# Performance work log

Hardware: AMD Instinct MI355X
Metric: run time of the kernel (lower is better)

The kernel has to match this reference:

```python
import jax, jax.numpy as jnp
import numpy as np

B, P, J, MOT, K, NB, WN, H = 64, 12273, 80, 94, 64, 20, 17, 128
W_POSE = 1.0

def euler_to_rotmat(a):
    # a: [..., 3] radians, R = Rz @ Ry @ Rx
    sx, sy, sz = jnp.sin(a[..., 0]), jnp.sin(a[..., 1]), jnp.sin(a[..., 2])
    cx, cy, cz = jnp.cos(a[..., 0]), jnp.cos(a[..., 1]), jnp.cos(a[..., 2])
    r00 = cz * cy; r01 = cz * sy * sx - sz * cx; r02 = cz * sy * cx + sz * sx
    r10 = sz * cy; r11 = sz * sy * sx + cz * cx; r12 = sz * sy * cx - cz * sx
    r20 = -sy;     r21 = cy * sx;                r22 = cy * cx
    return jnp.stack([jnp.stack([r00, r01, r02], -1),
                      jnp.stack([r10, r11, r12], -1),
                      jnp.stack([r20, r21, r22], -1)], -2)

def setup_inputs() -> dict:
    key = jax.random.key(0)
    ks = jax.random.split(key, 20)
    f32 = jnp.float32
    return {
        'in_pc_batch': jax.random.normal(ks[0], (B, P, 3), f32),
        't_nor': jax.random.normal(ks[1], (B, P, 3), f32),
        'rest_verts': jax.random.normal(ks[2], (P, 3), f32),
        'skin_weights': jax.random.uniform(ks[3], (P, J), f32),
        'mul_weight_list': jax.random.normal(ks[4], (J, MOT), f32),
        'query': jax.random.normal(ks[5], (B, J, 3), f32),
        'cloth_pose_std': jax.random.uniform(ks[6], (3,), f32),
        'cloth_pose_mean': jax.random.normal(ks[7], (3,), f32),
        'cloth_trans_std': jax.random.uniform(ks[8], (3,), f32),
        'cloth_trans_mean': jax.random.normal(ks[9], (3,), f32),
        'W1': jax.random.normal(ks[10], (3 + K, H), f32) * 0.1,
        'b1': jnp.zeros((H,), f32),
        'W2': jax.random.normal(ks[11], (H, 6), f32) * 0.1,
        'b2': jnp.zeros((6,), f32),
        'tmtemp': jax.random.normal(ks[12], (B, MOT, K), f32),
        'Wd': jax.random.normal(ks[13], (MOT * K, NB * WN), f32) * 0.02,
        'bd': jnp.zeros((NB * WN,), f32),
        'DPSD': jax.random.normal(ks[14], (NB, WN, P, 3), f32) * 0.1,
        'ssdr_res_std': jax.random.uniform(ks[15], (3,), f32),
        'ssdr_res_mean': jax.random.normal(ks[16], (3,), f32),
    }

def reference(in_pc_batch, t_nor, rest_verts, skin_weights, mul_weight_list,
              query, cloth_pose_std, cloth_pose_mean, cloth_trans_std,
              cloth_trans_mean, W1, b1, W2, b2, tmtemp, Wd, bd, DPSD,
              ssdr_res_std, ssdr_res_mean):
    # per-joint field input: [B, J, K]
    field_input = jnp.einsum('bjk,lj->blk', tmtemp, jax.nn.relu(mul_weight_list))
    # FieldNet: per-joint MLP on concat(query, field_input) -> [B, J, 6]
    h = jnp.concatenate([query, field_input], axis=-1)
    pred_rt = jax.nn.relu(h @ W1 + b1) @ W2 + b2
    pred_pose = pred_rt[..., 0:3] * cloth_pose_std + cloth_pose_mean
    pred_trans = (query + pred_rt[..., 3:6]) * cloth_trans_std + cloth_trans_mean
    # detailsnet + fused 20-basis accumulation: [B, P, 3]
    nbat = tmtemp.shape[0]
    detailkey = (tmtemp.reshape(nbat, -1) @ Wd + bd).reshape(nbat, NB, WN)
    detail_res = jnp.einsum('bnw,nwpx->bpx', detailkey, DPSD)
    detail_res = detail_res * ssdr_res_std + ssdr_res_mean
    # SSDR LBS skinning with Euler-angle rotations (degrees -> radians)
    R = euler_to_rotmat(jnp.deg2rad(pred_pose))            # [B, J, 3, 3]
    skinned = (jnp.einsum('pj,bjxy,py->bpx', skin_weights, R, rest_verts)
               + jnp.einsum('pj,bjx->bpx', skin_weights, pred_trans))
    out_pc = skinned + detail_res                          # [B, P, 3]
    loss_pose_l1 = jnp.mean(jnp.abs(in_pc_batch[:, :, 0:3] - out_pc))
    loss = loss_pose_l1 * W_POSE + 1e-4 * jnp.mean(DPSD ** 2)
    return loss[None], out_pc
```

## Files before the change

### kernel.cpp

```cpp
#include <hip/hip_runtime.h>

#define B_   64
#define P_   12273
#define J_   80
#define MOT_ 94
#define K_   64
#define H_   128
#define Q_   340
#define NE_  36819
#define MK_  6016
#define PW_  12288

typedef float v4f  __attribute__((ext_vector_type(4)));
typedef float v8f  __attribute__((ext_vector_type(8)));
typedef float v16f __attribute__((ext_vector_type(16)));
#define AS4 __attribute__((address_space(4)))

__device__ __forceinline__ const AS4 float* unif(const float* p){
  return (const AS4 float*)(unsigned long long)p;
}
__device__ __forceinline__ const AS4 v4f* univ4(const float* p){
  return (const AS4 v4f*)(unsigned long long)p;
}
__device__ __forceinline__ const AS4 v8f* univ8(const float* p){
  return (const AS4 v8f*)(unsigned long long)p;
}
__device__ __forceinline__ const AS4 v16f* univ16(const float* p){
  return (const AS4 v16f*)(unsigned long long)p;
}

__global__ __launch_bounds__(256) void k_prep(
    const float* __restrict__ query, const float* __restrict__ mwl,
    const float* __restrict__ tm,    const float* __restrict__ W1,
    const float* __restrict__ b1,    const float* __restrict__ W2,
    const float* __restrict__ b2,    const float* __restrict__ cps,
    const float* __restrict__ cpm,   const float* __restrict__ cts,
    const float* __restrict__ ctm,   const float* __restrict__ skin,
    float* __restrict__ G,           float* __restrict__ tm_t,
    float* __restrict__ w_t,         float* __restrict__ lacc)
{
  __shared__ float smem[80 * 65];
  int blk = blockIdx.x;
  int t = threadIdx.x;
  if (blk < 1280){
    int lane = t & 63;
    int wid = __builtin_amdgcn_readfirstlane(t >> 6);
    int bj = blk * 4 + wid;
    int b = bj / J_, l = bj - b * J_;
    float* hs = smem + wid * 80;
    float acc = 0.f;
    const AS4 float* mp = unif(mwl + l * MOT_);
    const float* tp = tm + (size_t)b * MK_ + lane;
    #pragma unroll 2
    for (int j = 0; j < MOT_; j++){
      float w = mp[j]; w = w > 0.f ? w : 0.f;
      acc = fmaf(w, tp[j * K_], acc);
    }
    hs[3 + lane] = acc;
    if (lane < 3) hs[lane] = query[(size_t)bj * 3 + lane];
    __syncthreads();
    float a1 = b1[lane], a2 = b1[lane + 64];
    for (int i = 0; i < 3 + K_; i++){
      float hv = hs[i];
      a1 = fmaf(hv, W1[i * H_ + lane], a1);
      a2 = fmaf(hv, W1[i * H_ + 64 + lane], a2);
    }
    a1 = a1 > 0.f ? a1 : 0.f;
    a2 = a2 > 0.f ? a2 : 0.f;
    const AS4 float* b2c = unif(b2);
    float rt[6];
    #pragma unroll
    for (int o = 0; o < 6; o++){
      float po = fmaf(a1, W2[lane * 6 + o], a2 * W2[(lane + 64) * 6 + o]);
      #pragma unroll
      for (int off = 32; off; off >>= 1) po += __shfl_xor(po, off);
      rt[o] = po + b2c[o];
    }
    const float D2R = 0.017453292519943295f;
    float ax = fmaf(rt[0], cps[0], cpm[0]) * D2R;
    float ay = fmaf(rt[1], cps[1], cpm[1]) * D2R;
    float az = fmaf(rt[2], cps[2], cpm[2]) * D2R;
    float tx = fmaf(hs[0] + rt[3], cts[0], ctm[0]);
    float ty = fmaf(hs[1] + rt[4], cts[1], ctm[1]);
    float tz = fmaf(hs[2] + rt[5], cts[2], ctm[2]);
    float sx, cx, sy, cy, sz, cz;
    sincosf(ax, &sx, &cx); sincosf(ay, &sy, &cy); sincosf(az, &sz, &cz);
    if (lane == 0){
      float4 r0 = make_float4(cz*cy, cz*sy*sx - sz*cx, cz*sy*cx + sz*sx, tx);
      float4 r1 = make_float4(sz*cy, sz*sy*sx + cz*cx, sz*sy*cx - cz*sx, ty);
      float4 r2 = make_float4(-sy,   cy*sx,            cy*cx,            tz);
      float4* g = (float4*)(G + (size_t)bj * 12);
      g[0] = r0; g[1] = r1; g[2] = r2;
    }
  } else if (blk < 1374){
    int m0 = (blk - 1280) * 64;
    int ml = t & 63, g = t >> 6;
    #pragma unroll
    for (int r = 0; r < 16; r++){
      int b = g * 16 + r;
      smem[ml * 65 + b] = tm[(size_t)b * MK_ + m0 + ml];
    }
    __syncthreads();
    int bl = t & 63;
    #pragma unroll
    for (int r = 0; r < 16; r++){
      int m = g * 16 + r;
      tm_t[(size_t)(m0 + m) * 64 + bl] = smem[m * 65 + bl];
    }
  } else if (blk < 1566){
    int p0 = (blk - 1374) * 64;
    #pragma unroll
    for (int k = 0; k < 20; k++){
      int idx = k * 256 + t;
      int pl = idx / 80, j = idx - pl * 80;
      int p = p0 + pl;
      smem[j * 65 + pl] = (p < P_) ? skin[(size_t)p * J_ + j] : 0.f;
    }
    __syncthreads();
    #pragma unroll
    for (int k = 0; k < 20; k++){
      int idx = k * 256 + t;
      int j = idx >> 6, pl = idx & 63;
      w_t[(size_t)j * PW_ + p0 + pl] = smem[j * 65 + pl];
    }
  } else {
    if (t < 2) lacc[t] = 0.f;
  }
}

__global__ __launch_bounds__(256) void k_dkey(
    const float* __restrict__ tm_t, const float* __restrict__ Wd,
    float* __restrict__ part)
{
  int t = threadIdx.x;
  int lane = t & 63;
  int wid = __builtin_amdgcn_readfirstlane(t >> 6);
  int qt = blockIdx.x;
  int q = qt * 64 + lane;
  bool vq = q < Q_;
  int m0 = blockIdx.y * 64;
  const AS4 v16f* tr = univ16(tm_t);
  float acc[16];
  #pragma unroll
  for (int i = 0; i < 16; i++) acc[i] = 0.f;
  float wbuf[4];
  #pragma unroll
  for (int i = 0; i < 4; i++)
    wbuf[i] = vq ? Wd[(size_t)(m0 + i) * Q_ + q] : 0.f;
  v16f tb0 = tr[(size_t)(m0 + 0) * 4 + wid];
  v16f tb1 = tr[(size_t)(m0 + 1) * 4 + wid];
  #pragma unroll 4
  for (int mm = 0; mm < 60; mm++){
    float wd = wbuf[mm & 3];
    wbuf[mm & 3] = vq ? Wd[(size_t)(m0 + mm + 4) * Q_ + q] : 0.f;
    v16f tv = tb0; tb0 = tb1;
    tb1 = tr[(size_t)(m0 + mm + 2) * 4 + wid];
    #pragma unroll
    for (int i = 0; i < 16; i++) acc[i] = fmaf(tv[i], wd, acc[i]);
  }
  #pragma unroll
  for (int mm = 60; mm < 64; mm++){
    float wd = wbuf[mm & 3];
    v16f tv = tb0; tb0 = tb1;
    if (mm < 62) tb1 = tr[(size_t)(m0 + mm + 2) * 4 + wid];
    #pragma unroll
    for (int i = 0; i < 16; i++) acc[i] = fmaf(tv[i], wd, acc[i]);
  }
  float* pb = part + ((size_t)blockIdx.y * 6 + qt) * 4096 + (size_t)(wid * 16) * 64;
  #pragma unroll
  for (int i = 0; i < 16; i++) pb[i * 64 + lane] = acc[i];
}

__global__ __launch_bounds__(256) void k_dkred(
    const float* __restrict__ part, const float* __restrict__ bd,
    float* __restrict__ dk_t, int S)
{
  int t = threadIdx.x;
  int jj = blockIdx.x * 32 + (t >> 3);
  int dl = t & 7;
  int b = jj / Q_, q = jj - b * Q_;
  int qt = q >> 6, ql = q & 63;
  const float* pp = part + (size_t)qt * 4096 + b * 64 + ql;
  float s = 0.f;
  for (int d = dl; d < S; d += 8) s += pp[(size_t)d * 6 * 4096];
  s += __shfl_xor(s, 1); s += __shfl_xor(s, 2); s += __shfl_xor(s, 4);
  if (dl == 0) dk_t[q * 64 + b] = bd[q] + s;
}

__device__ __forceinline__ void dconsume(const AS4 v16f* dkv, int qa, int wid,
                                         const float* dc, float* acc,
                                         float& sq, bool doSq)
{
  v16f r0 = dkv[(qa + 0) * 4 + wid];
  v16f r1 = dkv[(qa + 1) * 4 + wid];
  v16f r2 = dkv[(qa + 2) * 4 + wid];
  v16f r3 = dkv[(qa + 3) * 4 + wid];
  v16f r4 = dkv[(qa + 4) * 4 + wid];
  if (doSq){
    #pragma unroll
    for (int i = 0; i < 5; i++) sq = fmaf(dc[i], dc[i], sq);
  }
  #pragma unroll
  for (int i = 0; i < 16; i++){
    acc[i] = fmaf(r0[i], dc[0], acc[i]);
    acc[i] = fmaf(r1[i], dc[1], acc[i]);
    acc[i] = fmaf(r2[i], dc[2], acc[i]);
    acc[i] = fmaf(r3[i], dc[3], acc[i]);
    acc[i] = fmaf(r4[i], dc[4], acc[i]);
  }
}

__global__ __launch_bounds__(256) void k_detail(
    const float* __restrict__ DPSD, const float* __restrict__ dk_t,
    float* __restrict__ stg0, float* __restrict__ out,
    float* __restrict__ lacc, int qn)
{
  int t = threadIdx.x;
  int lane = t & 63;
  int wid = __builtin_amdgcn_readfirstlane(t >> 6);
  int b0 = wid * 16;
  int e = blockIdx.x * 64 + lane;
  bool ve = e < NE_;
  int q0 = blockIdx.y * qn;
  const AS4 v16f* dkv = univ16(dk_t);
  const float* Dp = DPSD + (ve ? e : 0);
  float acc[16];
  #pragma unroll
  for (int i = 0; i < 16; i++) acc[i] = 0.f;
  float sq = 0.f;
  bool doSq = (wid == 0);
  float da[5], db[5];
  #pragma unroll
  for (int i = 0; i < 5; i++) da[i] = Dp[(size_t)(q0 + i) * NE_];
  #pragma unroll
  for (int i = 0; i < 5; i++) db[i] = Dp[(size_t)(q0 + 5 + i) * NE_];
  int ng = qn / 5;
  int g = 0;
  for (; g + 2 < ng; g += 2){
    int qa = q0 + g * 5;
    float ta[5], tb[5];
    #pragma unroll
    for (int i = 0; i < 5; i++) ta[i] = Dp[(size_t)(qa + 10 + i) * NE_];
    dconsume(dkv, qa, wid, da, acc, sq, doSq);
    #pragma unroll
    for (int i = 0; i < 5; i++) da[i] = ta[i];
    #pragma unroll
    for (int i = 0; i < 5; i++) tb[i] = Dp[(size_t)(qa + 15 + i) * NE_];
    dconsume(dkv, qa + 5, wid, db, acc, sq, doSq);
    #pragma unroll
    for (int i = 0; i < 5; i++) db[i] = tb[i];
  }
  dconsume(dkv, q0 + (ng - 2) * 5, wid, da, acc, sq, doSq);
  dconsume(dkv, q0 + (ng - 1) * 5, wid, db, acc, sq, doSq);
  if (ve){
    bool toOut = (blockIdx.y + 1 == gridDim.y);
    float* dst = toOut ? (out + 1 + e) : (stg0 + e);
    #pragma unroll
    for (int i = 0; i < 16; i++)
      dst[(size_t)(b0 + i) * NE_] = acc[i];
  }
  if (doSq){
    if (!ve) sq = 0.f;
    #pragma unroll
    for (int off = 32; off; off >>= 1) sq += __shfl_xor(sq, off);
    if (lane == 0) atomicAdd(&lacc[1], sq);
  }
}

__global__ __launch_bounds__(256) void k_skin(
    const float* __restrict__ G, const float* __restrict__ w_t,
    const float* __restrict__ rest, const float* __restrict__ in_pc,
    const float* __restrict__ stg0, const float* __restrict__ rstd,
    const float* __restrict__ rmean,
    float* __restrict__ out, float* __restrict__ lacc, int two)
{
  int t = threadIdx.x;
  int lane = t & 63;
  int wid = __builtin_amdgcn_readfirstlane(t >> 6);
  int p  = blockIdx.x * 64 + lane;
  int bA = blockIdx.y * 8 + wid * 2;
  const AS4 v4f* gA = univ4(G + (size_t)bA * J_ * 12);
  const AS4 v4f* gB = univ4(G + ((size_t)bA + 1) * J_ * 12);
  float accA[12], accB[12];
  #pragma unroll
  for (int c = 0; c < 12; c++){ accA[c] = 0.f; accB[c] = 0.f; }
  const float* wp = w_t + p;
  #pragma unroll 4
  for (int j = 0; j < J_; j++){
    float w = wp[(size_t)j * PW_];
    v4f a0 = gA[j * 3 + 0], a1 = gA[j * 3 + 1], a2 = gA[j * 3 + 2];
    v4f c0 = gB[j * 3 + 0], c1 = gB[j * 3 + 1], c2 = gB[j * 3 + 2];
    #pragma unroll
    for (int c = 0; c < 4; c++){
      accA[c]     = fmaf(w, a0[c], accA[c]);
      accA[4 + c] = fmaf(w, a1[c], accA[4 + c]);
      accA[8 + c] = fmaf(w, a2[c], accA[8 + c]);
      accB[c]     = fmaf(w, c0[c], accB[c]);
      accB[4 + c] = fmaf(w, c1[c], accB[4 + c]);
      accB[8 + c] = fmaf(w, c2[c], accB[8 + c]);
    }
  }
  bool vp = p < P_;
  float vx = 0.f, vy = 0.f, vz = 0.f;
  if (vp){ vx = rest[p * 3]; vy = rest[p * 3 + 1]; vz = rest[p * 3 + 2]; }
  float srs[3], srm[3];
  #pragma unroll
  for (int x = 0; x < 3; x++){ srs[x] = rstd[x]; srm[x] = rmean[x]; }
  float lsum = 0.f;
  if (vp){
    size_t baseA = ((size_t)bA * P_ + p) * 3;
    size_t baseB = baseA + (size_t)P_ * 3;
    #pragma unroll
    for (int x = 0; x < 3; x++){
      float det = out[1 + baseA + x];
      if (two) det += stg0[baseA + x];
      float v = fmaf(accA[x*4+0], vx, fmaf(accA[x*4+1], vy, fmaf(accA[x*4+2], vz, accA[x*4+3])));
      v += fmaf(det, srs[x], srm[x]);
      lsum += fabsf(in_pc[baseA + x] - v);
      out[1 + baseA + x] = v;
    }
    #pragma unroll
    for (int x = 0; x < 3; x++){
      float det = out[1 + baseB + x];
      if (two) det += stg0[baseB + x];
      float v = fmaf(accB[x*4+0], vx, fmaf(accB[x*4+1], vy, fmaf(accB[x*4+2], vz, accB[x*4+3])));
      v += fmaf(det, srs[x], srm[x]);
      lsum += fabsf(in_pc[baseB + x] - v);
      out[1 + baseB + x] = v;
    }
  }
  #pragma unroll
  for (int off = 32; off; off >>= 1) lsum += __shfl_xor(lsum, off);
  __shared__ float red[4];
  if (lane == 0) red[wid] = lsum;
  __syncthreads();
  if (t == 0) atomicAdd(&lacc[0], red[0] + red[1] + red[2] + red[3]);
}

__global__ void k_finalize(const float* __restrict__ lacc, float* __restrict__ out){
  if (threadIdx.x == 0 && blockIdx.x == 0){
    float loss = lacc[0] * (1.f / 2356416.f) + 1e-4f * (lacc[1] * (1.f / 12518460.f));
    out[0] = loss;
  }
}

extern "C" void kernel_launch(void* const* d_in, const int* in_sizes, int n_in,
                              void* d_out, int out_size, void* d_ws, size_t ws_size,
                              hipStream_t stream){
  const float* in_pc = (const float*)d_in[0];
  const float* rest  = (const float*)d_in[2];
  const float* skin  = (const float*)d_in[3];
  const float* mwl   = (const float*)d_in[4];
  const float* query = (const float*)d_in[5];
  const float* cps   = (const float*)d_in[6];
  const float* cpm   = (const float*)d_in[7];
  const float* cts   = (const float*)d_in[8];
  const float* ctm   = (const float*)d_in[9];
  const float* W1    = (const float*)d_in[10];
  const float* b1    = (const float*)d_in[11];
  const float* W2    = (const float*)d_in[12];
  const float* b2    = (const float*)d_in[13];
  const float* tm    = (const float*)d_in[14];
  const float* Wd    = (const float*)d_in[15];
  const float* bd    = (const float*)d_in[16];
  const float* DPSD  = (const float*)d_in[17];
  const float* rstd  = (const float*)d_in[18];
  const float* rmean = (const float*)d_in[19];
  float* out = (float*)d_out;

  float* ws   = (float*)d_ws;
  float* G    = ws;
  float* dk_t = G + 61440;
  float* lacc = dk_t + 21760;
  float* tm_t = lacc + 64;
  float* w_t  = tm_t + 385024;
  float* un   = w_t + 983040;

  size_t have = ws_size / 4;
  int nqh = (have >= (size_t)(1451328 + 2356416)) ? 2 : 1;
  int qn = Q_ / nqh;

  k_prep    <<<1567, 256, 0, stream>>>(query, mwl, tm, W1, b1, W2, b2,
                                       cps, cpm, cts, ctm, skin,
                                       G, tm_t, w_t, lacc);
  k_dkey    <<<dim3(6, 94), 256, 0, stream>>>(tm_t, Wd, un);
  k_dkred   <<<680, 256, 0, stream>>>(un, bd, dk_t, 94);
  k_detail  <<<dim3(576, nqh), 256, 0, stream>>>(DPSD, dk_t, un, out, lacc, qn);
  k_skin    <<<dim3(192, 8), 256, 0, stream>>>(G, w_t, rest, in_pc, un, rstd, rmean,
                                               out, lacc, nqh - 1);
  k_finalize<<<1, 64, 0, stream>>>(lacc, out);
}
```

Before: 255.5 us.

## Relayout detail keys and rotation buffers; software-prefetch loads in prep MLP

Detail keys are now stored per 16-batch group, contiguous over q, so each wave in k_detail streams its slice with simpler scalar addressing. The per-joint transform buffer G interleaves batch pairs so k_skin reads both batches' matrices from one contiguous stream. In k_prep, the motion-weight and W1 loops use an 8-deep register prefetch ring to hide global load latency. Together these aim to cut address overhead and load stalls, at the cost of more registers and tighter coupling of layouts between kernels.

```diff
diff --git a/kernel.cpp b/kernel.cpp
--- a/kernel.cpp
+++ b/kernel.cpp
@@ -10,9 +10,9 @@
 #define NE_  36819
 #define MK_  6016
 #define PW_  12288
+#define STG_ 2356416
 
 typedef float v4f  __attribute__((ext_vector_type(4)));
-typedef float v8f  __attribute__((ext_vector_type(8)));
 typedef float v16f __attribute__((ext_vector_type(16)));
 #define AS4 __attribute__((address_space(4)))
 
@@ -21,9 +21,6 @@
 }
 __device__ __forceinline__ const AS4 v4f* univ4(const float* p){
   return (const AS4 v4f*)(unsigned long long)p;
-}
-__device__ __forceinline__ const AS4 v8f* univ8(const float* p){
-  return (const AS4 v8f*)(unsigned long long)p;
 }
 __device__ __forceinline__ const AS4 v16f* univ16(const float* p){
   return (const AS4 v16f*)(unsigned long long)p;
@@ -51,19 +48,36 @@
     float acc = 0.f;
     const AS4 float* mp = unif(mwl + l * MOT_);
     const float* tp = tm + (size_t)b * MK_ + lane;
-    #pragma unroll 2
+    float tbuf[8];
+    #pragma unroll
+    for (int s = 0; s < 8; s++) tbuf[s] = tp[s * K_];
+    #pragma unroll 8
     for (int j = 0; j < MOT_; j++){
+      float tv = tbuf[j & 7];
+      if (j + 8 < MOT_) tbuf[j & 7] = tp[(j + 8) * K_];
       float w = mp[j]; w = w > 0.f ? w : 0.f;
-      acc = fmaf(w, tp[j * K_], acc);
+      acc = fmaf(w, tv, acc);
     }
     hs[3 + lane] = acc;
     if (lane < 3) hs[lane] = query[(size_t)bj * 3 + lane];
     __syncthreads();
     float a1 = b1[lane], a2 = b1[lane + 64];
-    for (int i = 0; i < 3 + K_; i++){
+    float wa[8], wb[8];
+    #pragma unroll
+    for (int s = 0; s < 8; s++){
+      wa[s] = W1[s * H_ + lane];
+      wb[s] = W1[s * H_ + 64 + lane];
+    }
+    #pragma unroll 8
+    for (int i = 0; i < 67; i++){
       float hv = hs[i];
-      a1 = fmaf(hv, W1[i * H_ + lane], a1);
-      a2 = fmaf(hv, W1[i * H_ + 64 + lane], a2);
+      float va = wa[i & 7], vb = wb[i & 7];
+      if (i + 8 < 67){
+        wa[i & 7] = W1[(i + 8) * H_ + lane];
+        wb[i & 7] = W1[(i + 8) * H_ + 64 + lane];
+      }
+      a1 = fmaf(hv, va, a1);
+      a2 = fmaf(hv, vb, a2);
     }
     a1 = a1 > 0.f ? a1 : 0.f;
     a2 = a2 > 0.f ? a2 : 0.f;
@@ -89,7 +103,8 @@
       float4 r0 = make_float4(cz*cy, cz*sy*sx - sz*cx, cz*sy*cx + sz*sx, tx);
       float4 r1 = make_float4(sz*cy, sz*sy*sx + cz*cx, sz*sy*cx - cz*sx, ty);
       float4 r2 = make_float4(-sy,   cy*sx,            cy*cx,            tz);
-      float4* g = (float4*)(G + (size_t)bj * 12);
+      size_t o = ((size_t)(b >> 1) * J_ + l) * 24 + (b & 1) * 12;
+      float4* g = (float4*)(G + o);
       g[0] = r0; g[1] = r1; g[2] = r2;
     }
   } else if (blk < 1374){
@@ -173,7 +188,7 @@
 
 __global__ __launch_bounds__(256) void k_dkred(
     const float* __restrict__ part, const float* __restrict__ bd,
-    float* __restrict__ dk_t, int S)
+    float* __restrict__ dk_s, int S)
 {
   int t = threadIdx.x;
   int jj = blockIdx.x * 32 + (t >> 3);
@@ -184,18 +199,19 @@
   float s = 0.f;
   for (int d = dl; d < S; d += 8) s += pp[(size_t)d * 6 * 4096];
   s += __shfl_xor(s, 1); s += __shfl_xor(s, 2); s += __shfl_xor(s, 4);
-  if (dl == 0) dk_t[q * 64 + b] = bd[q] + s;
-}
-
-__device__ __forceinline__ void dconsume(const AS4 v16f* dkv, int qa, int wid,
-                                         const float* dc, float* acc,
-                                         float& sq, bool doSq)
-{
-  v16f r0 = dkv[(qa + 0) * 4 + wid];
-  v16f r1 = dkv[(qa + 1) * 4 + wid];
-  v16f r2 = dkv[(qa + 2) * 4 + wid];
-  v16f r3 = dkv[(qa + 3) * 4 + wid];
-  v16f r4 = dkv[(qa + 4) * 4 + wid];
+  if (dl == 0)
+    dk_s[(size_t)(b >> 4) * (Q_ * 16) + q * 16 + (b & 15)] = bd[q] + s;
+}
+
+__device__ __forceinline__ void dk_consume(const AS4 v16f* dkv, int qa,
+                                           const float* dc, float* acc,
+                                           float& sq, bool doSq)
+{
+  v16f r0 = dkv[qa + 0];
+  v16f r1 = dkv[qa + 1];
+  v16f r2 = dkv[qa + 2];
+  v16f r3 = dkv[qa + 3];
+  v16f r4 = dkv[qa + 4];
   if (doSq){
     #pragma unroll
     for (int i = 0; i < 5; i++) sq = fmaf(dc[i], dc[i], sq);
@@ -211,8 +227,8 @@
 }
 
 __global__ __launch_bounds__(256) void k_detail(
-    const float* __restrict__ DPSD, const float* __restrict__ dk_t,
-    float* __restrict__ stg0, float* __restrict__ out,
+    const float* __restrict__ DPSD, const float* __restrict__ dk_s,
+    float* __restrict__ stg, float* __restrict__ out,
     float* __restrict__ lacc, int qn)
 {
   int t = threadIdx.x;
@@ -222,39 +238,38 @@
   int e = blockIdx.x * 64 + lane;
   bool ve = e < NE_;
   int q0 = blockIdx.y * qn;
-  const AS4 v16f* dkv = univ16(dk_t);
+  const AS4 v16f* dkv = univ16(dk_s + (size_t)wid * (Q_ * 16));
   const float* Dp = DPSD + (ve ? e : 0);
   float acc[16];
   #pragma unroll
   for (int i = 0; i < 16; i++) acc[i] = 0.f;
   float sq = 0.f;
   bool doSq = (wid == 0);
+  int ng = qn / 5;
   float da[5], db[5];
   #pragma unroll
   for (int i = 0; i < 5; i++) da[i] = Dp[(size_t)(q0 + i) * NE_];
   #pragma unroll
   for (int i = 0; i < 5; i++) db[i] = Dp[(size_t)(q0 + 5 + i) * NE_];
-  int ng = qn / 5;
-  int g = 0;
-  for (; g + 2 < ng; g += 2){
+  for (int g = 0; g + 2 < ng; g += 2){
     int qa = q0 + g * 5;
     float ta[5], tb[5];
     #pragma unroll
     for (int i = 0; i < 5; i++) ta[i] = Dp[(size_t)(qa + 10 + i) * NE_];
-    dconsume(dkv, qa, wid, da, acc, sq, doSq);
+    dk_consume(dkv, qa, da, acc, sq, doSq);
     #pragma unroll
     for (int i = 0; i < 5; i++) da[i] = ta[i];
     #pragma unroll
     for (int i = 0; i < 5; i++) tb[i] = Dp[(size_t)(qa + 15 + i) * NE_];
-    dconsume(dkv, qa + 5, wid, db, acc, sq, doSq);
+    dk_consume(dkv, qa + 5, db, acc, sq, doSq);
     #pragma unroll
     for (int i = 0; i < 5; i++) db[i] = tb[i];
   }
-  dconsume(dkv, q0 + (ng - 2) * 5, wid, da, acc, sq, doSq);
-  dconsume(dkv, q0 + (ng - 1) * 5, wid, db, acc, sq, doSq);
+  dk_consume(dkv, q0 + (ng - 2) * 5, da, acc, sq, doSq);
+  dk_consume(dkv, q0 + (ng - 1) * 5, db, acc, sq, doSq);
   if (ve){
     bool toOut = (blockIdx.y + 1 == gridDim.y);
-    float* dst = toOut ? (out + 1 + e) : (stg0 + e);
+    float* dst = toOut ? (out + 1 + e) : (stg + e);
     #pragma unroll
     for (int i = 0; i < 16; i++)
       dst[(size_t)(b0 + i) * NE_] = acc[i];
@@ -270,7 +285,7 @@
 __global__ __launch_bounds__(256) void k_skin(
     const float* __restrict__ G, const float* __restrict__ w_t,
     const float* __restrict__ rest, const float* __restrict__ in_pc,
-    const float* __restrict__ stg0, const float* __restrict__ rstd,
+    const float* __restrict__ stg, const float* __restrict__ rstd,
     const float* __restrict__ rmean,
     float* __restrict__ out, float* __restrict__ lacc, int two)
 {
@@ -279,8 +294,8 @@
   int wid = __builtin_amdgcn_readfirstlane(t >> 6);
   int p  = blockIdx.x * 64 + lane;
   int bA = blockIdx.y * 8 + wid * 2;
-  const AS4 v4f* gA = univ4(G + (size_t)bA * J_ * 12);
-  const AS4 v4f* gB = univ4(G + ((size_t)bA + 1) * J_ * 12);
+  int bp = (blockIdx.y * 4 + wid);
+  const AS4 v4f* gS = univ4(G + (size_t)bp * J_ * 24);
   float accA[12], accB[12];
   #pragma unroll
   for (int c = 0; c < 12; c++){ accA[c] = 0.f; accB[c] = 0.f; }
@@ -288,8 +303,8 @@
   #pragma unroll 4
   for (int j = 0; j < J_; j++){
     float w = wp[(size_t)j * PW_];
-    v4f a0 = gA[j * 3 + 0], a1 = gA[j * 3 + 1], a2 = gA[j * 3 + 2];
-    v4f c0 = gB[j * 3 + 0], c1 = gB[j * 3 + 1], c2 = gB[j * 3 + 2];
+    v4f a0 = gS[j * 6 + 0], a1 = gS[j * 6 + 1], a2 = gS[j * 6 + 2];
+    v4f c0 = gS[j * 6 + 3], c1 = gS[j * 6 + 4], c2 = gS[j * 6 + 5];
     #pragma unroll
     for (int c = 0; c < 4; c++){
       accA[c]     = fmaf(w, a0[c], accA[c]);
@@ -313,7 +328,7 @@
     #pragma unroll
     for (int x = 0; x < 3; x++){
       float det = out[1 + baseA + x];
-      if (two) det += stg0[baseA + x];
+      if (two) det += stg[baseA + x];
       float v = fmaf(accA[x*4+0], vx, fmaf(accA[x*4+1], vy, fmaf(accA[x*4+2], vz, accA[x*4+3])));
       v += fmaf(det, srs[x], srm[x]);
       lsum += fabsf(in_pc[baseA + x] - v);
@@ -322,7 +337,7 @@
     #pragma unroll
     for (int x = 0; x < 3; x++){
       float det = out[1 + baseB + x];
-      if (two) det += stg0[baseB + x];
+      if (two) det += stg[baseB + x];
       float v = fmaf(accB[x*4+0], vx, fmaf(accB[x*4+1], vy, fmaf(accB[x*4+2], vz, accB[x*4+3])));
       v += fmaf(det, srs[x], srm[x]);
       lsum += fabsf(in_pc[baseB + x] - v);
@@ -370,8 +385,8 @@
 
   float* ws   = (float*)d_ws;
   float* G    = ws;
-  float* dk_t = G + 61440;
-  float* lacc = dk_t + 21760;
+  float* dk_s = G + 61440;
+  float* lacc = dk_s + 21760;
   float* tm_t = lacc + 64;
   float* w_t  = tm_t + 385024;
   float* un   = w_t + 983040;
@@ -384,8 +399,8 @@
                                        cps, cpm, cts, ctm, skin,
                                        G, tm_t, w_t, lacc);
   k_dkey    <<<dim3(6, 94), 256, 0, stream>>>(tm_t, Wd, un);
-  k_dkred   <<<680, 256, 0, stream>>>(un, bd, dk_t, 94);
-  k_detail  <<<dim3(576, nqh), 256, 0, stream>>>(DPSD, dk_t, un, out, lacc, qn);
+  k_dkred   <<<680, 256, 0, stream>>>(un, bd, dk_s, 94);
+  k_detail  <<<dim3(576, nqh), 256, 0, stream>>>(DPSD, dk_s, un, out, lacc, qn);
   k_skin    <<<dim3(192, 8), 256, 0, stream>>>(G, w_t, rest, in_pc, un, rstd, rmean,
                                                out, lacc, nqh - 1);
   k_finalize<<<1, 64, 0, stream>>>(lacc, out);
```

Result: slower. 286.1 us (+12.0%).
